# Optimization experiments

Hardware: AMD Instinct MI355X
Metric: run time of the kernel (lower is better)

The kernel has to match this reference:

```python
import jax, jax.numpy as jnp
import numpy as np
from math import sqrt

D_MODEL, N_H, D_H, D_CQ, D_CKV, D_HR = 2048, 16, 128, 768, 512, 64
B, S = 1, 2048


def _rope_cos_sin(seq_len, dim, base=10000.0):
    inv_freq = 1.0 / (base ** (jnp.arange(0, dim, 2, dtype=jnp.float32) / dim))
    ang = jnp.arange(seq_len, dtype=jnp.float32)[:, None] * inv_freq[None, :]  # (S, dim//2)
    return jnp.cos(ang), jnp.sin(ang)


def _rope(t, cos, sin):
    # t: (B, S, ..., dim) with sequence on axis 1; interleaved complex pairs
    shp = t.shape
    d2 = shp[-1] // 2
    tr = t.reshape(shp[:-1] + (d2, 2))
    x0, x1 = tr[..., 0], tr[..., 1]
    bshape = (1, shp[1]) + (1,) * (x0.ndim - 3) + (d2,)
    cs, sn = cos.reshape(bshape), sin.reshape(bshape)
    return jnp.stack([x0 * cs - x1 * sn, x0 * sn + x1 * cs], axis=-1).reshape(shp)


def setup_inputs() -> dict:
    key = jax.random.key(0)
    ks = jax.random.split(key, 10)
    sc = 0.02
    inp = {
        "x": jax.random.normal(ks[0], (B, S, D_MODEL), jnp.float32),
        "mask": jnp.triu(jnp.ones((S, S), dtype=bool), k=1),  # True -> masked (causal)
        "w_norm": jnp.ones((D_MODEL,), jnp.float32),
        "w_cq": jax.random.normal(ks[1], (D_MODEL, D_CQ), jnp.float32) * sc,
        "w_q": jax.random.normal(ks[2], (D_CQ, N_H * D_H), jnp.float32) * sc,
        "w_qr": jax.random.normal(ks[3], (D_CQ, N_H * D_HR), jnp.float32) * sc,
        "w_ckv": jax.random.normal(ks[4], (D_MODEL, D_CKV), jnp.float32) * sc,
        "w_k": jax.random.normal(ks[5], (D_CKV, N_H * D_H), jnp.float32) * sc,
        "w_kr": jax.random.normal(ks[6], (D_MODEL, D_HR), jnp.float32) * sc,
        "w_v": jax.random.normal(ks[7], (D_CKV, D_MODEL), jnp.float32) * sc,
        "w_o": jax.random.normal(ks[8], (N_H * D_H, D_MODEL), jnp.float32) * sc,
    }
    return inp


def reference(x, mask, w_norm, w_cq, w_q, w_qr, w_ckv, w_k, w_kr, w_v, w_o):
    b, s, _ = x.shape
    eps = jnp.finfo(x.dtype).eps
    h = x * jax.lax.rsqrt(jnp.mean(x * x, axis=-1, keepdims=True) + eps) * w_norm  # RMSNorm
    cos, sin = _rope_cos_sin(s, D_HR)

    c_q = h @ w_cq  # (b, s, d_c_q)
    q_c = (c_q @ w_q).reshape(b, s, N_H, D_H).transpose(0, 2, 1, 3)          # (b, h, s, d_h)
    q_r = _rope((c_q @ w_qr).reshape(b, s, N_H, D_HR), cos, sin).transpose(0, 2, 1, 3)
    q = jnp.concatenate([q_c, q_r], axis=-1)  # (b, h, s, d_h + d_h_R)

    c_kv = h @ w_ckv  # (b, s, d_c_kv)
    k_c = (c_kv @ w_k).reshape(b, s, N_H, D_H).transpose(0, 2, 1, 3)
    k_r = _rope(h @ w_kr, cos, sin)[:, None]  # (b, 1, s, d_h_R), shared across heads
    k = jnp.concatenate([k_c, jnp.broadcast_to(k_r, (b, N_H, s, D_HR))], axis=-1)
    v = (c_kv @ w_v).reshape(b, s, N_H, D_H).transpose(0, 2, 1, 3)

    score = jnp.einsum('bhqd,bhkd->bhqk', q, k) / sqrt(D_H + D_HR)
    score = jnp.where(mask, -jnp.inf, score)
    attn = jax.nn.softmax(score, axis=-1)
    out = jnp.einsum('bhqk,bhkd->bhqd', attn, v)  # (b, h, s, d_h)
    out = out.transpose(0, 2, 1, 3).reshape(b, s, N_H * D_H) @ w_o
    return x + out
```

## Files before the change

### kernel.cpp

```cpp
#include <hip/hip_runtime.h>
#include <hip/hip_bf16.h>
#include <math.h>

#define D_MODEL 2048
#define N_H     16
#define D_H     128
#define D_CQ    768
#define D_CKV   512
#define D_HR    64
#define SEQ     2048
#define N_ACT1  1408
#define NSPLIT  4
#define ATT_SCALE 0.07216878364870323f

typedef short bf16x8 __attribute__((ext_vector_type(8)));
typedef short short4v __attribute__((ext_vector_type(4)));
typedef float f32x4  __attribute__((ext_vector_type(4)));

__device__ inline short f2bf(float f) {
  union { float f; unsigned u; } v; v.f = f;
  unsigned r = (v.u + 0x7fff + ((v.u >> 16) & 1)) >> 16;
  return (short)r;
}
__device__ inline float bf2f(short s) {
  union { float f; unsigned u; } v; v.u = ((unsigned)(unsigned short)s) << 16;
  return v.f;
}

__device__ inline void gld_lds16(const void* g, void* l) {
#if __has_builtin(__builtin_amdgcn_global_load_lds)
  __builtin_amdgcn_global_load_lds(
      (const __attribute__((address_space(1))) unsigned int*)g,
      (__attribute__((address_space(3))) unsigned int*)l, 16, 0, 0);
#else
  int lane = threadIdx.x & 63;
  *((uint4*)l + lane) = *(const uint4*)g;
#endif
}

struct CastJobs {
  const float* src[8];
  short* dst[8];
  int K[8];
  int pref[9];
  int nx[8];
};

__global__ __launch_bounds__(256) void prep_all(
    CastJobs J, const float* __restrict__ x, const float* __restrict__ wn,
    short* __restrict__ hb) {
  int bid = blockIdx.x;
  int tid = threadIdx.x;

  if (bid >= J.pref[8]) {
    int row = bid - J.pref[8];
    const float* xr = x + (size_t)row * D_MODEL;
    float ss = 0.f;
    for (int i = tid; i < D_MODEL; i += 256) { float v = xr[i]; ss += v * v; }
    __shared__ float red[256];
    red[tid] = ss;
    __syncthreads();
    for (int s = 128; s > 0; s >>= 1) {
      if (tid < s) red[tid] += red[tid + s];
      __syncthreads();
    }
    float scale = rsqrtf(red[0] / (float)D_MODEL + 1.1920929e-7f);
    short* hbr = hb + (size_t)row * D_MODEL;
    for (int i = tid; i < D_MODEL; i += 256) hbr[i] = f2bf(xr[i] * scale * wn[i]);
    return;
  }

  int j = 0;
#pragma unroll
  for (int t = 0; t < 8; t++)
    if (bid >= J.pref[t + 1]) j = t + 1;
  int lid = bid - J.pref[j];
  int nx = J.nx[j];
  int ty = lid / nx, tx = lid - ty * nx;
  int n0 = tx * 64, k0 = ty * 64;
  int K = J.K[j];
  const float* W = J.src[j];
  short* Wt = J.dst[j];
  int Nfull = nx * 64;

  __shared__ short T[64][68];
#pragma unroll
  for (int it = 0; it < 16; it++) {
    int idx = it * 256 + tid;
    int r = idx >> 6, c = idx & 63;
    T[c][r] = f2bf(W[(size_t)(k0 + r) * Nfull + n0 + c]);
  }
  __syncthreads();
#pragma unroll
  for (int it = 0; it < 16; it++) {
    int idx = it * 256 + tid;
    int r = idx >> 6, c = idx & 63;
    Wt[(size_t)(n0 + r) * K + k0 + c] = T[r][c];
  }
}

__device__ __forceinline__ void gemm64_body(
    const short* __restrict__ A, const short* __restrict__ Bt,
    short* __restrict__ Cb, short* __restrict__ Cb2,
    int M, int N, int K, int lda, int ldb,
    int mode, int bxx, int byy) {
  __shared__ short As[2 * 64 * 64];
  __shared__ short Bs[2 * 128 * 64];
  int tid = threadIdx.x;
  int w = tid >> 6, l = tid & 63;
  int lq = l >> 4, l16 = l & 15;
  int bm = byy * 64, bn = bxx * 128;
  int wr = w >> 1, wc = w & 1;
  int wm0 = wr * 32, wn0 = wc * 64;

  f32x4 acc[2][4];
#pragma unroll
  for (int i = 0; i < 2; i++)
#pragma unroll
    for (int j = 0; j < 4; j++) acc[i][j] = (f32x4)0.f;

  int rsub = (l >> 3);
  int csub = ((l & 7) ^ rsub) << 3;

  auto stage = [&](int buf, int k0) {
    short* Asb = As + buf * (64 * 64);
    short* Bsb = Bs + buf * (128 * 64);
#pragma unroll
    for (int i = 0; i < 2; i++) {
      int r0 = i * 32 + w * 8;
      gld_lds16(A + (size_t)(bm + r0 + rsub) * lda + k0 + csub, Asb + r0 * 64);
    }
#pragma unroll
    for (int i = 0; i < 4; i++) {
      int r0 = i * 32 + w * 8;
      gld_lds16(Bt + (size_t)(bn + r0 + rsub) * ldb + k0 + csub, Bsb + r0 * 64);
    }
  };

  stage(0, 0);
  int cur = 0;
  for (int k0 = 0; k0 < K; k0 += 64) {
    __syncthreads();
    if (k0 + 64 < K) stage(cur ^ 1, k0 + 64);
    const short* Asb = As + cur * (64 * 64);
    const short* Bsb = Bs + cur * (128 * 64);

#pragma unroll
    for (int ks = 0; ks < 2; ks++) {
      bf16x8 af[2], bfr[4];
      int sw = ((ks * 4 + lq) ^ (l16 & 7)) << 3;
#pragma unroll
      for (int mt = 0; mt < 2; mt++)
        af[mt] = *(const bf16x8*)&Asb[(wm0 + mt * 16 + l16) * 64 + sw];
#pragma unroll
      for (int nt = 0; nt < 4; nt++)
        bfr[nt] = *(const bf16x8*)&Bsb[(wn0 + nt * 16 + l16) * 64 + sw];
#pragma unroll
      for (int mt = 0; mt < 2; mt++)
#pragma unroll
        for (int nt = 0; nt < 4; nt++)
          acc[mt][nt] = __builtin_amdgcn_mfma_f32_16x16x32_bf16(af[mt], bfr[nt], acc[mt][nt], 0, 0, 0);
    }
    cur ^= 1;
  }

#pragma unroll
  for (int mt = 0; mt < 2; mt++)
#pragma unroll
    for (int nt = 0; nt < 4; nt++) {
      int col = bn + wn0 + nt * 16 + l16;
      int row0 = bm + wm0 + mt * 16 + lq * 4;
      if (mode == 4 && col >= 2048) {
        int cc = col - 2048;
        short4v v4;
#pragma unroll
        for (int i = 0; i < 4; i++) v4[i] = f2bf(acc[mt][nt][i]);
        *(short4v*)&Cb2[(size_t)cc * SEQ + row0] = v4;
        continue;
      }
#pragma unroll
      for (int i = 0; i < 4; i++) {
        int row = row0 + i;
        float v = acc[mt][nt][i];
        if (mode == 3) {
          if (col < 2048) {
            Cb[((size_t)(col >> 7) * M + row) * 192 + (col & 127)] =
                f2bf(v * ATT_SCALE);
          } else {
            int cc = col - 2048;
            int hh = cc >> 6, dd = cc & 63;
            float partner = __shfl_xor(v, 1);
            float inv = __expf(-((float)(dd & ~1) / 64.0f) * 9.210340372f);
            float ang = (float)row * inv;
            float c = __cosf(ang), s = __sinf(ang);
            float res = ((dd & 1) == 0) ? (v * c - partner * s)
                                        : (partner * s + v * c);
            Cb[((size_t)hh * M + row) * 192 + 128 + dd] = f2bf(res * ATT_SCALE);
          }
        } else {
          Cb[((size_t)(col >> 7) * M + row) * 192 + (col & 127)] = f2bf(v);
        }
      }
    }
}

__global__ __launch_bounds__(256) void gemm_qkv(
    const short* __restrict__ act1, const short* __restrict__ WT2,
    const short* __restrict__ WT3, short* __restrict__ qb,
    short* __restrict__ kb, short* __restrict__ vt) {
  int bx = blockIdx.x;
  if (bx < 24) {
    gemm64_body(act1, WT2, qb, nullptr,
                SEQ, 3072, D_CQ, N_ACT1, D_CQ, 3, bx, blockIdx.y);
  } else {
    gemm64_body(act1 + 768, WT3, kb, vt,
                SEQ, 4096, D_CKV, N_ACT1, D_CKV, 4, bx - 24, blockIdx.y);
  }
}

__global__ __launch_bounds__(256, 4) void gemm_bf16_6464(
    const short* __restrict__ A, const short* __restrict__ Bt,
    float* __restrict__ Cf, short* __restrict__ Cb,
    const float* __restrict__ addv, int M, int N, int K, int lda, int ldb,
    int mode) {
  __shared__ short As[2 * 64 * 64];
  __shared__ short Bs[2 * 64 * 64];
  int tid = threadIdx.x;
  int w = tid >> 6, l = tid & 63;
  int lq = l >> 4, l16 = l & 15;
  int bm = blockIdx.y * 64, bn = blockIdx.x * 64;
  int wr = w >> 1, wc = w & 1;
  int wm0 = wr * 32, wn0 = wc * 32;

  f32x4 acc[2][2];
#pragma unroll
  for (int i = 0; i < 2; i++)
#pragma unroll
    for (int j = 0; j < 2; j++) acc[i][j] = (f32x4)0.f;

  int rsub = (l >> 3);
  int csub = ((l & 7) ^ rsub) << 3;

  auto stage = [&](int buf, int k0) {
    short* Asb = As + buf * (64 * 64);
    short* Bsb = Bs + buf * (64 * 64);
#pragma unroll
    for (int i = 0; i < 2; i++) {
      int r0 = i * 32 + w * 8;
      gld_lds16(A + (size_t)(bm + r0 + rsub) * lda + k0 + csub, Asb + r0 * 64);
      gld_lds16(Bt + (size_t)(bn + r0 + rsub) * ldb + k0 + csub, Bsb + r0 * 64);
    }
  };

  stage(0, 0);
  int cur = 0;
  for (int k0 = 0; k0 < K; k0 += 64) {
    __syncthreads();
    if (k0 + 64 < K) stage(cur ^ 1, k0 + 64);
    const short* Asb = As + cur * (64 * 64);
    const short* Bsb = Bs + cur * (64 * 64);

#pragma unroll
    for (int ks = 0; ks < 2; ks++) {
      bf16x8 af[2], bfr[2];
      int sw = ((ks * 4 + lq) ^ (l16 & 7)) << 3;
#pragma unroll
      for (int mt = 0; mt < 2; mt++)
        af[mt] = *(const bf16x8*)&Asb[(wm0 + mt * 16 + l16) * 64 + sw];
#pragma unroll
      for (int nt = 0; nt < 2; nt++)
        bfr[nt] = *(const bf16x8*)&Bsb[(wn0 + nt * 16 + l16) * 64 + sw];
#pragma unroll
      for (int mt = 0; mt < 2; mt++)
#pragma unroll
        for (int nt = 0; nt < 2; nt++)
          acc[mt][nt] = __builtin_amdgcn_mfma_f32_16x16x32_bf16(af[mt], bfr[nt], acc[mt][nt], 0, 0, 0);
    }
    cur ^= 1;
  }

#pragma unroll
  for (int mt = 0; mt < 2; mt++)
#pragma unroll
    for (int nt = 0; nt < 2; nt++) {
      int col = bn + wn0 + nt * 16 + l16;
      int row0 = bm + wm0 + mt * 16 + lq * 4;
#pragma unroll
      for (int i = 0; i < 4; i++) {
        int row = row0 + i;
        float v = acc[mt][nt][i];
        if (mode == 0) {
          size_t off = (size_t)row * N + col;
          if (addv) v += addv[off];
          Cf[off] = v;
        } else {
          Cb[(size_t)row * N + col] = f2bf(v);
        }
      }
    }
}

__global__ void rope_k_kernel(const short* __restrict__ act1, short* __restrict__ kb) {
  int idx = blockIdx.x * blockDim.x + threadIdx.x;
  if (idx >= SEQ * 32) return;
  int j = idx & 31;
  int s = idx >> 5;
  const short* p = act1 + (size_t)s * N_ACT1 + 1280 + 2 * j;
  float x0 = bf2f(p[0]), x1 = bf2f(p[1]);
  float inv = __expf(-((float)(2 * j) / 64.0f) * 9.210340372f);
  float ang = (float)s * inv;
  float c = __cosf(ang), sn = __sinf(ang);
  short b0 = f2bf(x0 * c - x1 * sn);
  short b1 = f2bf(x0 * sn + x1 * c);
#pragma unroll
  for (int hh = 0; hh < N_H; hh++) {
    short* k = kb + ((size_t)hh * SEQ + s) * 192 + 128 + 2 * j;
    k[0] = b0;
    k[1] = b1;
  }
}

#define TQ 128
#define TK 64
#define KSZ (TK * 192)

__global__ __launch_bounds__(256, 2) void attn_mfma(
    const short* __restrict__ qb, const short* __restrict__ kb,
    const short* __restrict__ vt, short* __restrict__ Opart,
    float* __restrict__ Lpart) {
  int bid = blockIdx.x;
  int h = bid & 15;
  int rest = bid >> 4;
  int qt = 15 - (rest / NSPLIT);
  int split = rest % NSPLIT;
  int q0 = qt * TQ;
  int nk = 2 * (qt + 1);
  int tid = threadIdx.x;
  int wave = tid >> 6, lane = tid & 63;
  int lq = lane >> 4, l16 = lane & 15;

  __shared__ short Ks[2 * KSZ];
  __shared__ short Vs[128 * 64];
  __shared__ short Ps[TQ * 64];

  bf16x8 qf[2][6];
  {
    const short* qp = qb + ((size_t)h * SEQ + q0 + wave * 32 + l16) * 192;
#pragma unroll
    for (int mt = 0; mt < 2; mt++)
#pragma unroll
      for (int ks = 0; ks < 6; ks++)
        qf[mt][ks] = *(const bf16x8*)(qp + (size_t)mt * 16 * 192 + ks * 32 + lq * 8);
  }

  bf16x8 ones;
#pragma unroll
  for (int i = 0; i < 8; i++) ones[i] = (short)0x3F80;

  f32x4 O[2][8];
  f32x4 Ol[2];
#pragma unroll
  for (int mt = 0; mt < 2; mt++) {
    Ol[mt] = (f32x4)0.f;
#pragma unroll
    for (int i = 0; i < 8; i++) O[mt][i] = (f32x4)0.f;
  }

  int goffK[6];
#pragma unroll
  for (int i = 0; i < 6; i++) {
    int s = i * 256 + tid;
    int r = s / 24;
    int c = s - r * 24;
    goffK[i] = r * 192 + ((c ^ (r & 7)) << 3);
  }
  int goffV[4];
  int vrow[4];
#pragma unroll
  for (int i = 0; i < 4; i++) {
    int s = i * 256 + tid;
    int d = s >> 3;
    int p = s & 7;
    vrow[i] = d;
    goffV[i] = (p ^ (d & 7)) << 3;
  }
  const short* kb_h = kb + (size_t)h * SEQ * 192;
  const short* vt_h = vt + (size_t)h * 128 * SEQ;

  auto stage_k = [&](int k0s, int buf) {
#pragma unroll
    for (int i = 0; i < 6; i++)
      gld_lds16(kb_h + (size_t)k0s * 192 + goffK[i],
                Ks + buf * KSZ + (size_t)(i * 256 + wave * 64) * 8);
  };
  auto stage_v = [&](int k0s) {
#pragma unroll
    for (int i = 0; i < 4; i++)
      gld_lds16(vt_h + (size_t)vrow[i] * SEQ + k0s + goffV[i],
                Vs + (size_t)(i * 256 + wave * 64) * 8);
  };

  if (split < nk) stage_k(split * TK, 0);
  int kbuf = 0;

  for (int t = split; t < nk; t += NSPLIT) {
    int k0 = t * TK;
    __syncthreads();

    stage_v(k0);
    if (t + NSPLIT < nk) stage_k((t + NSPLIT) * TK, kbuf ^ 1);

    const short* Ksb = Ks + kbuf * KSZ;
    f32x4 S[2][4];
#pragma unroll
    for (int mt = 0; mt < 2; mt++)
#pragma unroll
      for (int nt = 0; nt < 4; nt++) S[mt][nt] = (f32x4)0.f;
    __builtin_amdgcn_s_setprio(1);
#pragma unroll
    for (int ks = 0; ks < 6; ks++) {
#pragma unroll
      for (int nt = 0; nt < 4; nt++) {
        int row = nt * 16 + l16;
        bf16x8 b = *(const bf16x8*)&Ksb[row * 192 +
                                        (((ks * 4 + lq) ^ (l16 & 7)) << 3)];
#pragma unroll
        for (int mt = 0; mt < 2; mt++)
          S[mt][nt] = __builtin_amdgcn_mfma_f32_16x16x32_bf16(qf[mt][ks], b, S[mt][nt], 0, 0, 0);
      }
    }
    __builtin_amdgcn_s_setprio(0);

#pragma unroll
    for (int mt = 0; mt < 2; mt++)
#pragma unroll
      for (int i = 0; i < 4; i++) {
        int pr = wave * 32 + mt * 16 + lq * 4 + i;
        int row = q0 + pr;
        bool may = (k0 + 63 > row);
#pragma unroll
        for (int nt = 0; nt < 4; nt++) {
          float p;
          if (may && (k0 + nt * 16 + l16 > row)) p = 0.f;
          else p = __expf(S[mt][nt][i]);
          int j = nt * 16 + l16;
          Ps[pr * 64 + ((((j >> 3) ^ (pr & 7)) << 3) | (j & 7))] = f2bf(p);
        }
      }

    __syncthreads();

    __builtin_amdgcn_s_setprio(1);
#pragma unroll
    for (int kh = 0; kh < 2; kh++) {
      bf16x8 a[2];
#pragma unroll
      for (int mt = 0; mt < 2; mt++) {
        int prw = wave * 32 + mt * 16 + l16;
        a[mt] = *(const bf16x8*)&Ps[prw * 64 +
                                    (((kh * 4 + lq) ^ (l16 & 7)) << 3)];
        Ol[mt] = __builtin_amdgcn_mfma_f32_16x16x32_bf16(a[mt], ones, Ol[mt], 0, 0, 0);
      }
#pragma unroll
      for (int nt = 0; nt < 8; nt++) {
        int d = nt * 16 + l16;
        bf16x8 b = *(const bf16x8*)&Vs[d * 64 +
                                       (((kh * 4 + lq) ^ (d & 7)) << 3)];
#pragma unroll
        for (int mt = 0; mt < 2; mt++)
          O[mt][nt] = __builtin_amdgcn_mfma_f32_16x16x32_bf16(a[mt], b, O[mt][nt], 0, 0, 0);
      }
    }
    __builtin_amdgcn_s_setprio(0);
    kbuf ^= 1;
  }

#pragma unroll
  for (int mt = 0; mt < 2; mt++)
#pragma unroll
    for (int i = 0; i < 4; i++) {
      int row = q0 + wave * 32 + mt * 16 + lq * 4 + i;
      size_t base = ((size_t)(split * N_H + h) * SEQ + row);
      size_t obase = base * 128;
#pragma unroll
      for (int nt = 0; nt < 8; nt++)
        Opart[obase + nt * 16 + l16] = f2bf(O[mt][nt][i]);
      if (l16 == 0) Lpart[base] = Ol[mt][i];
    }
}

__global__ __launch_bounds__(256) void attn_merge(
    const short* __restrict__ Opart, const float* __restrict__ Lpart,
    short* __restrict__ aob) {
  int q0 = blockIdx.x * 16;
  int h = blockIdx.y;
  int tid = threadIdx.x;
#pragma unroll
  for (int i = 0; i < 8; i++) {
    int c = i * 256 + tid;
    int row = q0 + (c >> 7), d = c & 127;
    float denom = 0.f, num = 0.f;
#pragma unroll
    for (int p = 0; p < NSPLIT; p++) {
      size_t base = (size_t)(p * N_H + h) * SEQ + row;
      denom += Lpart[base];
      num += bf2f(Opart[base * 128 + d]);
    }
    aob[(size_t)row * D_MODEL + h * 128 + d] = f2bf(num / denom);
  }
}

extern "C" void kernel_launch(void* const* d_in, const int* in_sizes, int n_in,
                              void* d_out, int out_size, void* d_ws, size_t ws_size,
                              hipStream_t stream) {
  const float* x      = (const float*)d_in[0];
  const float* w_norm = (const float*)d_in[2];
  const float* w_cq   = (const float*)d_in[3];
  const float* w_q    = (const float*)d_in[4];
  const float* w_qr   = (const float*)d_in[5];
  const float* w_ckv  = (const float*)d_in[6];
  const float* w_k    = (const float*)d_in[7];
  const float* w_kr   = (const float*)d_in[8];
  const float* w_v    = (const float*)d_in[9];
  const float* w_o    = (const float*)d_in[10];
  float* out = (float*)d_out;

  char* ws = (char*)d_ws;
  short* h_bf  = (short*)ws;  ws += (size_t)SEQ * D_MODEL * 2;
  short* act1  = (short*)ws;  ws += (size_t)SEQ * N_ACT1 * 2;
  short* qb    = (short*)ws;  ws += (size_t)N_H * SEQ * 192 * 2;
  short* kb    = (short*)ws;  ws += (size_t)N_H * SEQ * 192 * 2;
  short* vt    = (short*)ws;  ws += (size_t)SEQ * D_MODEL * 2;
  short* ao_bf = (short*)ws;  ws += (size_t)SEQ * D_MODEL * 2;
  short* Opart = (short*)ws;  ws += (size_t)NSPLIT * N_H * SEQ * 128 * 2;
  float* Lpart = (float*)ws;  ws += (size_t)NSPLIT * N_H * SEQ * 4;
  short* WT1   = (short*)ws;  ws += (size_t)N_ACT1 * D_MODEL * 2;
  short* WT2   = (short*)ws;  ws += (size_t)3072 * D_CQ * 2;
  short* WT3   = (short*)ws;  ws += (size_t)4096 * D_CKV * 2;
  short* WTO   = (short*)ws;  ws += (size_t)D_MODEL * D_MODEL * 2;

  CastJobs J;
  J.src[0] = w_cq;  J.dst[0] = WT1;                              J.K[0] = D_MODEL; J.nx[0] = D_CQ / 64;
  J.src[1] = w_ckv; J.dst[1] = WT1 + (size_t)768 * D_MODEL;      J.K[1] = D_MODEL; J.nx[1] = D_CKV / 64;
  J.src[2] = w_kr;  J.dst[2] = WT1 + (size_t)1280 * D_MODEL;     J.K[2] = D_MODEL; J.nx[2] = D_HR / 64;
  J.src[3] = w_q;   J.dst[3] = WT2;                              J.K[3] = D_CQ;    J.nx[3] = 2048 / 64;
  J.src[4] = w_qr;  J.dst[4] = WT2 + (size_t)2048 * D_CQ;        J.K[4] = D_CQ;    J.nx[4] = 1024 / 64;
  J.src[5] = w_k;   J.dst[5] = WT3;                              J.K[5] = D_CKV;   J.nx[5] = 2048 / 64;
  J.src[6] = w_v;   J.dst[6] = WT3 + (size_t)2048 * D_CKV;       J.K[6] = D_CKV;   J.nx[6] = 2048 / 64;
  J.src[7] = w_o;   J.dst[7] = WTO;                              J.K[7] = D_MODEL; J.nx[7] = 2048 / 64;
  int pref = 0;
  for (int j = 0; j < 8; j++) {
    J.pref[j] = pref;
    pref += J.nx[j] * (J.K[j] / 64);
  }
  J.pref[8] = pref;
  prep_all<<<pref + SEQ, 256, 0, stream>>>(J, x, w_norm, h_bf);

  gemm_bf16_6464<<<dim3(N_ACT1 / 64, SEQ / 64), 256, 0, stream>>>(
      h_bf, WT1, nullptr, act1, nullptr, SEQ, N_ACT1, D_MODEL,
      D_MODEL, D_MODEL, 1);

  rope_k_kernel<<<(SEQ * 32 + 255) / 256, 256, 0, stream>>>(act1, kb);

  gemm_qkv<<<dim3(24 + 32, SEQ / 64), 256, 0, stream>>>(
      act1, WT2, WT3, qb, kb, vt);

  attn_mfma<<<dim3((SEQ / TQ) * NSPLIT * N_H), 256, 0, stream>>>(qb, kb, vt, Opart, Lpart);
  attn_merge<<<dim3(SEQ / 16, N_H), 256, 0, stream>>>(Opart, Lpart, ao_bf);

  gemm_bf16_6464<<<dim3(D_MODEL / 64, SEQ / 64), 256, 0, stream>>>(
      ao_bf, WTO, out, nullptr, x, SEQ, D_MODEL, D_MODEL,
      D_MODEL, D_MODEL, 0);
}
```

Baseline: 266.0 us.

## Fuse rope-K into QKV GEMM and split-K merge into attention via atomic counter

The standalone RoPE-K kernel becomes an extra block column of the QKV GEMM launch, and the separate attention-merge kernel is replaced by a last-arriving-block merge inside the attention kernel. A per-(head, q-tile) atomic counter, zeroed in the prep kernel, elects the block that combines the split partials with vectorized 16-byte loads and stores. This removes two kernel launches and their inter-kernel gaps. In exchange it adds threadfence and atomic traffic, and the merge work now runs serially in the tail blocks of the attention kernel.

```diff
diff --git a/kernel.cpp b/kernel.cpp
--- a/kernel.cpp
+++ b/kernel.cpp
@@ -48,9 +48,11 @@
 
 __global__ __launch_bounds__(256) void prep_all(
     CastJobs J, const float* __restrict__ x, const float* __restrict__ wn,
-    short* __restrict__ hb) {
+    short* __restrict__ hb, int* __restrict__ cnt) {
   int bid = blockIdx.x;
   int tid = threadIdx.x;
+
+  if (bid == 0) cnt[tid] = 0;
 
   if (bid >= J.pref[8]) {
     int row = bid - J.pref[8];
@@ -209,6 +211,30 @@
     const short* __restrict__ WT3, short* __restrict__ qb,
     short* __restrict__ kb, short* __restrict__ vt) {
   int bx = blockIdx.x;
+  if (bx == 56) {
+    int s0 = blockIdx.y * 64;
+    int tid = threadIdx.x;
+#pragma unroll
+    for (int it = 0; it < 8; it++) {
+      int idx = it * 256 + tid;
+      int j = idx & 31;
+      int s = s0 + (idx >> 5);
+      const short* p = act1 + (size_t)s * N_ACT1 + 1280 + 2 * j;
+      float x0 = bf2f(p[0]), x1 = bf2f(p[1]);
+      float inv = __expf(-((float)(2 * j) / 64.0f) * 9.210340372f);
+      float ang = (float)s * inv;
+      float c = __cosf(ang), sn = __sinf(ang);
+      short b0 = f2bf(x0 * c - x1 * sn);
+      short b1 = f2bf(x0 * sn + x1 * c);
+#pragma unroll
+      for (int hh = 0; hh < N_H; hh++) {
+        short* k = kb + ((size_t)hh * SEQ + s) * 192 + 128 + 2 * j;
+        k[0] = b0;
+        k[1] = b1;
+      }
+    }
+    return;
+  }
   if (bx < 24) {
     gemm64_body(act1, WT2, qb, nullptr,
                 SEQ, 3072, D_CQ, N_ACT1, D_CQ, 3, bx, blockIdx.y);
@@ -300,26 +326,6 @@
     }
 }
 
-__global__ void rope_k_kernel(const short* __restrict__ act1, short* __restrict__ kb) {
-  int idx = blockIdx.x * blockDim.x + threadIdx.x;
-  if (idx >= SEQ * 32) return;
-  int j = idx & 31;
-  int s = idx >> 5;
-  const short* p = act1 + (size_t)s * N_ACT1 + 1280 + 2 * j;
-  float x0 = bf2f(p[0]), x1 = bf2f(p[1]);
-  float inv = __expf(-((float)(2 * j) / 64.0f) * 9.210340372f);
-  float ang = (float)s * inv;
-  float c = __cosf(ang), sn = __sinf(ang);
-  short b0 = f2bf(x0 * c - x1 * sn);
-  short b1 = f2bf(x0 * sn + x1 * c);
-#pragma unroll
-  for (int hh = 0; hh < N_H; hh++) {
-    short* k = kb + ((size_t)hh * SEQ + s) * 192 + 128 + 2 * j;
-    k[0] = b0;
-    k[1] = b1;
-  }
-}
-
 #define TQ 128
 #define TK 64
 #define KSZ (TK * 192)
@@ -327,7 +333,8 @@
 __global__ __launch_bounds__(256, 2) void attn_mfma(
     const short* __restrict__ qb, const short* __restrict__ kb,
     const short* __restrict__ vt, short* __restrict__ Opart,
-    float* __restrict__ Lpart) {
+    float* __restrict__ Lpart, short* __restrict__ aob,
+    int* __restrict__ cnt) {
   int bid = blockIdx.x;
   int h = bid & 15;
   int rest = bid >> 4;
@@ -487,26 +494,40 @@
         Opart[obase + nt * 16 + l16] = f2bf(O[mt][nt][i]);
       if (l16 == 0) Lpart[base] = Ol[mt][i];
     }
-}
-
-__global__ __launch_bounds__(256) void attn_merge(
-    const short* __restrict__ Opart, const float* __restrict__ Lpart,
-    short* __restrict__ aob) {
-  int q0 = blockIdx.x * 16;
-  int h = blockIdx.y;
-  int tid = threadIdx.x;
-#pragma unroll
-  for (int i = 0; i < 8; i++) {
-    int c = i * 256 + tid;
-    int row = q0 + (c >> 7), d = c & 127;
-    float denom = 0.f, num = 0.f;
+
+  __threadfence();
+  __syncthreads();
+  __shared__ int lastflag;
+  if (tid == 0) {
+    int old = atomicAdd(&cnt[h * 16 + qt], 1);
+    lastflag = (old == NSPLIT - 1) ? 1 : 0;
+  }
+  __syncthreads();
+  if (!lastflag) return;
+  __threadfence();
+
+#pragma unroll
+  for (int it = 0; it < 8; it++) {
+    int c = it * 256 + tid;
+    int rr = c >> 4;
+    int ch = c & 15;
+    int row = q0 + rr;
+    float den = 0.f;
+    float num[8];
+#pragma unroll
+    for (int j = 0; j < 8; j++) num[j] = 0.f;
 #pragma unroll
     for (int p = 0; p < NSPLIT; p++) {
       size_t base = (size_t)(p * N_H + h) * SEQ + row;
-      denom += Lpart[base];
-      num += bf2f(Opart[base * 128 + d]);
-    }
-    aob[(size_t)row * D_MODEL + h * 128 + d] = f2bf(num / denom);
+      den += Lpart[base];
+      bf16x8 o = *(const bf16x8*)&Opart[base * 128 + ch * 8];
+#pragma unroll
+      for (int j = 0; j < 8; j++) num[j] += bf2f(o[j]);
+    }
+    bf16x8 res;
+#pragma unroll
+    for (int j = 0; j < 8; j++) res[j] = f2bf(num[j] / den);
+    *(bf16x8*)&aob[(size_t)row * D_MODEL + h * 128 + ch * 8] = res;
   }
 }
 
@@ -534,6 +555,7 @@
   short* ao_bf = (short*)ws;  ws += (size_t)SEQ * D_MODEL * 2;
   short* Opart = (short*)ws;  ws += (size_t)NSPLIT * N_H * SEQ * 128 * 2;
   float* Lpart = (float*)ws;  ws += (size_t)NSPLIT * N_H * SEQ * 4;
+  int*   cnt   = (int*)ws;    ws += 256 * 4;
   short* WT1   = (short*)ws;  ws += (size_t)N_ACT1 * D_MODEL * 2;
   short* WT2   = (short*)ws;  ws += (size_t)3072 * D_CQ * 2;
   short* WT3   = (short*)ws;  ws += (size_t)4096 * D_CKV * 2;
@@ -554,19 +576,17 @@
     pref += J.nx[j] * (J.K[j] / 64);
   }
   J.pref[8] = pref;
-  prep_all<<<pref + SEQ, 256, 0, stream>>>(J, x, w_norm, h_bf);
+  prep_all<<<pref + SEQ, 256, 0, stream>>>(J, x, w_norm, h_bf, cnt);
 
   gemm_bf16_6464<<<dim3(N_ACT1 / 64, SEQ / 64), 256, 0, stream>>>(
       h_bf, WT1, nullptr, act1, nullptr, SEQ, N_ACT1, D_MODEL,
       D_MODEL, D_MODEL, 1);
 
-  rope_k_kernel<<<(SEQ * 32 + 255) / 256, 256, 0, stream>>>(act1, kb);
-
-  gemm_qkv<<<dim3(24 + 32, SEQ / 64), 256, 0, stream>>>(
+  gemm_qkv<<<dim3(24 + 32 + 1, SEQ / 64), 256, 0, stream>>>(
       act1, WT2, WT3, qb, kb, vt);
 
-  attn_mfma<<<dim3((SEQ / TQ) * NSPLIT * N_H), 256, 0, stream>>>(qb, kb, vt, Opart, Lpart);
-  attn_merge<<<dim3(SEQ / 16, N_H), 256, 0, stream>>>(Opart, Lpart, ao_bf);
+  attn_mfma<<<dim3((SEQ / TQ) * NSPLIT * N_H), 256, 0, stream>>>(
+      qb, kb, vt, Opart, Lpart, ao_bf, cnt);
 
   gemm_bf16_6464<<<dim3(D_MODEL / 64, SEQ / 64), 256, 0, stream>>>(
       ao_bf, WTO, out, nullptr, x, SEQ, D_MODEL, D_MODEL,
```

Result: slower. 461.0 us (+73.3%).
